# Optimization experiments

Measured on AMD Instinct MI355X. Metric: run time of the kernel, lower is better.

## Reference

```python
import jax, jax.numpy as jnp
import numpy as np

B, T, DIM, HEADS = 8, 1024, 256, 8
DH = DIM // HEADS


def setup_inputs() -> dict:
    key = jax.random.key(0)
    ks = jax.random.split(key, 8)
    x = jax.random.normal(ks[0], (B, T, DIM), dtype=jnp.float32)
    adj = jax.random.randint(ks[1], (B, 1, T, T), 0, 2).astype(jnp.int32)
    label = jax.random.randint(ks[2], (B,), 0, 10).astype(jnp.int64)
    Wq = jax.random.normal(ks[3], (DH, DH), dtype=jnp.float32) * 0.05
    Wk = jax.random.normal(ks[4], (DH, DH), dtype=jnp.float32) * 0.05
    Wv = jax.random.normal(ks[5], (DH, DH), dtype=jnp.float32) * 0.05
    Lam = jax.random.normal(ks[6], (HEADS, HEADS), dtype=jnp.float32)
    Wproj = jax.random.normal(ks[7], (DIM, DIM), dtype=jnp.float32) * 0.05
    return dict(x=x, adj=adj, label=label, Wq=Wq, Wk=Wk, Wv=Wv, Lam=Lam, Wproj=Wproj)


def reference(x, adj, label, Wq, Wk, Wv, Lam, Wproj):
    b, t, dim = x.shape
    h, dh = HEADS, dim // HEADS
    scale = dim ** (-0.5)  # note: scale uses full dim, as in the source
    # b t (h d) -> b h t d
    xh = x.reshape(b, t, h, dh).transpose(0, 2, 1, 3)
    adj_f = adj.astype(x.dtype)  # [b,1,t,t], broadcasts over heads

    def gcn(W, A):
        # graph conv: A @ (x @ W), per-head, weight shared across heads
        return jnp.matmul(A, jnp.einsum('bhtd,de->bhte', xh, W))

    q = gcn(Wq, adj_f)  # [b,h,t,dh]
    k = gcn(Wk, adj_f)
    attn = jnp.einsum('bhld,bhtd->bhlt', q, k) * scale
    attn = jax.nn.leaky_relu(attn, negative_slope=0.01)
    # cross-head Lambda mixing: new_head_i = sum_j Lam[i,j] * attn_head_j
    attn = jnp.einsum('ij,bjlt->bilt', Lam, attn)
    # layer_index=0 < depth//4=3 -> adjacency masking is active
    attn = jnp.where(adj > 0, attn, -jnp.inf)
    attn = jax.nn.softmax(attn, axis=-1)  # rep_adj [b,h,t,t]
    v = jnp.matmul(attn, jnp.einsum('bhtd,de->bhte', xh, Wv))  # GCN with attn as adjacency
    v = v.transpose(0, 2, 1, 3).reshape(b, t, dim)  # b h t d -> b t (h d)
    v = jax.nn.gelu(v, approximate=False)
    out = v @ Wproj.T  # nn.Linear, no bias
    return out, attn
```

## Files before the change

### kernel.cpp

```cpp
#include <hip/hip_runtime.h>
#include <cmath>

#define TT 1024
#define BB 8

typedef __attribute__((ext_vector_type(4))) float f4;
typedef __attribute__((ext_vector_type(4))) unsigned int u4;
typedef __attribute__((ext_vector_type(8))) short s8v;

__device__ __forceinline__ ushort f2bf(float x) {
  unsigned u = __builtin_bit_cast(unsigned, x);
  unsigned r = (u + 0x7FFFu + ((u >> 16) & 1u)) >> 16;
  return (ushort)r;
}
__device__ __forceinline__ float bf2f(ushort b) {
  unsigned u = ((unsigned)b) << 16;
  return __builtin_bit_cast(float, u);
}
__device__ __forceinline__ void st8(ushort* p, const ushort* v) {
  u4 w;
  w.x = (unsigned)v[0] | ((unsigned)v[1] << 16);
  w.y = (unsigned)v[2] | ((unsigned)v[3] << 16);
  w.z = (unsigned)v[4] | ((unsigned)v[5] << 16);
  w.w = (unsigned)v[6] | ((unsigned)v[7] << 16);
  *(u4*)p = w;
}

__global__ __launch_bounds__(256, 1) void k_xw(
    const float* __restrict__ x, const float* __restrict__ Wq,
    const float* __restrict__ Wk, const float* __restrict__ Wv,
    ushort* __restrict__ xTqhi, ushort* __restrict__ xTqlo,
    ushort* __restrict__ xTkhi, ushort* __restrict__ xTklo,
    ushort* __restrict__ vT) {
  __shared__ float xs[32][256];
  int bid = blockIdx.x;
  int b = bid & 7, t0 = (bid >> 3) * 32;
  int tid = threadIdx.x;
#pragma unroll
  for (int i = 0; i < 8; ++i) {
    int e = i * 256 + tid;
    int t = e >> 6, c4 = (e & 63) * 4;
    *(f4*)&xs[t][c4] = *(const f4*)&x[((size_t)(b * 1024 + t0 + t)) * 256 + c4];
  }
  int c = tid, h = c >> 5, d = c & 31;
  float wqr[32], wkr[32], wvr[32];
#pragma unroll
  for (int e = 0; e < 32; ++e) {
    wqr[e] = Wq[e * 32 + d] * 0.0625f;
    wkr[e] = Wk[e * 32 + d];
    wvr[e] = Wv[e * 32 + d];
  }
  __syncthreads();
  size_t rowq = ((size_t)(b * 256 + c)) * 1024 + t0;
#pragma unroll
  for (int tg = 0; tg < 4; ++tg) {
    ushort qh[8], ql[8], kh[8], kl[8], vh[8];
#pragma unroll
    for (int tt = 0; tt < 8; ++tt) {
      int t = tg * 8 + tt;
      float aq = 0.f, ak = 0.f, av = 0.f;
#pragma unroll
      for (int e = 0; e < 32; ++e) {
        float xe = xs[t][h * 32 + e];
        aq = fmaf(xe, wqr[e], aq);
        ak = fmaf(xe, wkr[e], ak);
        av = fmaf(xe, wvr[e], av);
      }
      ushort hq = f2bf(aq); qh[tt] = hq; ql[tt] = f2bf(aq - bf2f(hq));
      ushort hk = f2bf(ak); kh[tt] = hk; kl[tt] = f2bf(ak - bf2f(hk));
      vh[tt] = f2bf(av);
    }
    st8(xTqhi + rowq + tg * 8, qh);
    st8(xTqlo + rowq + tg * 8, ql);
    st8(xTkhi + rowq + tg * 8, kh);
    st8(xTklo + rowq + tg * 8, kl);
    st8(vT    + rowq + tg * 8, vh);
  }
}

__global__ __launch_bounds__(256, 1) void k_gcn(
    const int* __restrict__ adj,
    const ushort* __restrict__ xTqhi, const ushort* __restrict__ xTqlo,
    const ushort* __restrict__ xTkhi, const ushort* __restrict__ xTklo,
    ushort* __restrict__ qhi, ushort* __restrict__ qlo,
    ushort* __restrict__ khi, ushort* __restrict__ klo) {
  int bid = blockIdx.x;
  int b = bid & 7, r = bid >> 3;
  int lt = (r & 15) * 64, nt = r >> 4;
  const ushort* XH = (nt ? xTkhi : xTqhi) + (size_t)b * 256 * 1024;
  const ushort* XL = (nt ? xTklo : xTqlo) + (size_t)b * 256 * 1024;
  ushort* OH = (nt ? khi : qhi) + (size_t)b * 1024 * 256;
  ushort* OL = (nt ? klo : qlo) + (size_t)b * 1024 * 256;
  const int* AD = adj + (size_t)b * 1024 * 1024;
  int tid = threadIdx.x, wid = tid >> 6, lane = tid & 63;
  int lrow = lane & 15, lk = lane >> 4;
  int wr = wid >> 1, wc = wid & 1;
  int rbase = lt + wr * 32;
  int cbase = wc * 128;
  f4 acc[2][8];
#pragma unroll
  for (int i = 0; i < 2; ++i)
#pragma unroll
    for (int j = 0; j < 8; ++j) acc[i][j] = (f4)(0.f);

  for (int k0 = 0; k0 < 1024; k0 += 32) {
    s8v afr[2];
#pragma unroll
    for (int rq = 0; rq < 2; ++rq) {
      const int* ap = &AD[(size_t)(rbase + rq * 16 + lrow) * 1024 + k0 + lk * 8];
      int4 a0 = *(const int4*)ap;
      int4 a1 = *(const int4*)(ap + 4);
      u4 fw;
      fw.x = (a0.x ? 0x3F80u : 0u) | (a0.y ? 0x3F800000u : 0u);
      fw.y = (a0.z ? 0x3F80u : 0u) | (a0.w ? 0x3F800000u : 0u);
      fw.z = (a1.x ? 0x3F80u : 0u) | (a1.y ? 0x3F800000u : 0u);
      fw.w = (a1.z ? 0x3F80u : 0u) | (a1.w ? 0x3F800000u : 0u);
      afr[rq] = __builtin_bit_cast(s8v, fw);
    }
#pragma unroll
    for (int nq = 0; nq < 8; ++nq) {
      int col = cbase + nq * 16 + lrow;
      s8v bh = *(const s8v*)&XH[(size_t)col * 1024 + k0 + lk * 8];
      s8v bl = *(const s8v*)&XL[(size_t)col * 1024 + k0 + lk * 8];
#pragma unroll
      for (int rq = 0; rq < 2; ++rq) {
        acc[rq][nq] = __builtin_amdgcn_mfma_f32_16x16x32_bf16(afr[rq], bh, acc[rq][nq], 0, 0, 0);
        acc[rq][nq] = __builtin_amdgcn_mfma_f32_16x16x32_bf16(afr[rq], bl, acc[rq][nq], 0, 0, 0);
      }
    }
  }
#pragma unroll
  for (int rq = 0; rq < 2; ++rq)
#pragma unroll
    for (int nq = 0; nq < 8; ++nq)
#pragma unroll
      for (int e = 0; e < 4; ++e) {
        float v = acc[rq][nq][e];
        int row = rbase + rq * 16 + lk * 4 + e;
        int col = cbase + nq * 16 + lrow;
        ushort hi = f2bf(v);
        ushort lo = f2bf(v - bf2f(hi));
        OH[(size_t)row * 256 + col] = hi;
        OL[(size_t)row * 256 + col] = lo;
      }
}

__global__ __launch_bounds__(256, 1) void k_score(
    const ushort* __restrict__ qhi, const ushort* __restrict__ qlo,
    const ushort* __restrict__ khi, const ushort* __restrict__ klo,
    const int* __restrict__ adj, const float* __restrict__ Lam,
    float* __restrict__ attn) {
  __shared__ float sm_m[2][32][8];
  __shared__ float sm_s[2][32][8];
  __shared__ float fin_m[32][8];
  __shared__ float fin_r[32][8];
  int bid = blockIdx.x;
  int b = bid & 7, lt = (bid >> 3) * 32;
  int tid = threadIdx.x, wid = tid >> 6, lane = tid & 63;
  int lrow = lane & 15, lk = lane >> 4;
  int wr = wid >> 1, wc = wid & 1;
  const ushort* QH = qhi + (size_t)b * 1024 * 256;
  const ushort* QL = qlo + (size_t)b * 1024 * 256;
  const ushort* KH = khi + (size_t)b * 1024 * 256;
  const ushort* KL = klo + (size_t)b * 1024 * 256;
  const int* AD = adj + (size_t)b * 1024 * 1024;
  float* AT = attn + (size_t)b * 8 * 1024 * 1024;

  s8v qfh[8], qfl[8];
  int qrow = lt + wr * 16 + lrow;
#pragma unroll
  for (int h = 0; h < 8; ++h) {
    qfh[h] = *(const s8v*)&QH[(size_t)qrow * 256 + h * 32 + lk * 8];
    qfl[h] = *(const s8v*)&QL[(size_t)qrow * 256 + h * 32 + lk * 8];
  }
  float ms[4][8], ss[4][8];
#pragma unroll
  for (int e = 0; e < 4; ++e)
#pragma unroll
    for (int i2 = 0; i2 < 8; ++i2) { ms[e][i2] = -3.0e38f; ss[e][i2] = 0.f; }

  for (int it = 0; it < 32; ++it) {
    int t0 = (it * 2 + wc) * 16;
    f4 acc[8];
#pragma unroll
    for (int h = 0; h < 8; ++h) {
      s8v kh = *(const s8v*)&KH[(size_t)(t0 + lrow) * 256 + h * 32 + lk * 8];
      s8v kl = *(const s8v*)&KL[(size_t)(t0 + lrow) * 256 + h * 32 + lk * 8];
      f4 a = (f4)(0.f);
      a = __builtin_amdgcn_mfma_f32_16x16x32_bf16(qfh[h], kh, a, 0, 0, 0);
      a = __builtin_amdgcn_mfma_f32_16x16x32_bf16(qfh[h], kl, a, 0, 0, 0);
      a = __builtin_amdgcn_mfma_f32_16x16x32_bf16(qfl[h], kh, a, 0, 0, 0);
      acc[h] = a;
    }
#pragma unroll
    for (int e = 0; e < 4; ++e) {
      int row = lt + wr * 16 + lk * 4 + e;
      int a = AD[(size_t)row * 1024 + t0 + lrow];
      bool pred = a > 0;
      float raw[8];
#pragma unroll
      for (int h = 0; h < 8; ++h) { float v = acc[h][e]; raw[h] = fmaxf(v, 0.01f * v); }
#pragma unroll
      for (int i2 = 0; i2 < 8; ++i2) {
        float s = 0.f;
#pragma unroll
        for (int j = 0; j < 8; ++j) s = fmaf(Lam[i2 * 8 + j], raw[j], s);
        float d = s - ms[e][i2];
        float ex = __expf(fminf(d, -d));
        float snew = (d > 0.f) ? fmaf(ss[e][i2], ex, 1.f) : (ss[e][i2] + ex);
        float mnew = fmaxf(ms[e][i2], s);
        if (pred) { ss[e][i2] = snew; ms[e][i2] = mnew; }
      }
    }
  }
#pragma unroll
  for (int e = 0; e < 4; ++e)
#pragma unroll
    for (int i2 = 0; i2 < 8; ++i2) {
      float mm = ms[e][i2], sv = ss[e][i2];
      for (int off = 1; off < 16; off <<= 1) {
        float om = __shfl_xor(mm, off, 64);
        float os = __shfl_xor(sv, off, 64);
        float d = mm - om;
        float ex = __expf(fminf(d, -d));
        float sA = fmaf(os, ex, sv);
        float sB = fmaf(sv, ex, os);
        sv = (d >= 0.f) ? sA : sB;
        mm = fmaxf(mm, om);
      }
      ms[e][i2] = mm; ss[e][i2] = sv;
    }
  if (lrow == 0) {
#pragma unroll
    for (int e = 0; e < 4; ++e)
#pragma unroll
      for (int i2 = 0; i2 < 8; ++i2) {
        sm_m[wc][wr * 16 + lk * 4 + e][i2] = ms[e][i2];
        sm_s[wc][wr * 16 + lk * 4 + e][i2] = ss[e][i2];
      }
  }
  __syncthreads();
  {
    int rw = tid >> 3, i2 = tid & 7;
    float m0 = sm_m[0][rw][i2], m1 = sm_m[1][rw][i2];
    float s0 = sm_s[0][rw][i2], s1 = sm_s[1][rw][i2];
    float M = fmaxf(m0, m1);
    float S = s0 * __expf(m0 - M) + s1 * __expf(m1 - M);
    fin_m[rw][i2] = M;
    fin_r[rw][i2] = 1.f / S;
  }
  __syncthreads();
#pragma unroll
  for (int e = 0; e < 4; ++e)
#pragma unroll
    for (int i2 = 0; i2 < 8; ++i2) {
      ms[e][i2] = fin_m[wr * 16 + lk * 4 + e][i2];
      ss[e][i2] = fin_r[wr * 16 + lk * 4 + e][i2];
    }
  for (int it = 0; it < 32; ++it) {
    int t0 = (it * 2 + wc) * 16;
    f4 acc[8];
#pragma unroll
    for (int h = 0; h < 8; ++h) {
      s8v kh = *(const s8v*)&KH[(size_t)(t0 + lrow) * 256 + h * 32 + lk * 8];
      s8v kl = *(const s8v*)&KL[(size_t)(t0 + lrow) * 256 + h * 32 + lk * 8];
      f4 a = (f4)(0.f);
      a = __builtin_amdgcn_mfma_f32_16x16x32_bf16(qfh[h], kh, a, 0, 0, 0);
      a = __builtin_amdgcn_mfma_f32_16x16x32_bf16(qfh[h], kl, a, 0, 0, 0);
      a = __builtin_amdgcn_mfma_f32_16x16x32_bf16(qfl[h], kh, a, 0, 0, 0);
      acc[h] = a;
    }
#pragma unroll
    for (int e = 0; e < 4; ++e) {
      int row = lt + wr * 16 + lk * 4 + e;
      int a = AD[(size_t)row * 1024 + t0 + lrow];
      bool pred = a > 0;
      float raw[8];
#pragma unroll
      for (int h = 0; h < 8; ++h) { float v = acc[h][e]; raw[h] = fmaxf(v, 0.01f * v); }
#pragma unroll
      for (int i2 = 0; i2 < 8; ++i2) {
        float s = 0.f;
#pragma unroll
        for (int j = 0; j < 8; ++j) s = fmaf(Lam[i2 * 8 + j], raw[j], s);
        float p = pred ? __expf(s - ms[e][i2]) * ss[e][i2] : 0.f;
        AT[((size_t)i2 * 1024 + row) * 1024 + t0 + lrow] = p;
      }
    }
  }
}

__global__ __launch_bounds__(256, 4) void k_pv(
    const float* __restrict__ attn, const ushort* __restrict__ vT,
    float* __restrict__ g) {
  __shared__ ushort Vs[32][136];
  __shared__ unsigned pt[64 * 128 / 2];
  int bid = blockIdx.x;
  int b = bid & 7, h = (bid >> 3) & 7, lt = (bid >> 6) * 64;
  int tid = threadIdx.x, wid = tid >> 6, lane = tid & 63;
  int lrow = lane & 15, lk = lane >> 4;
  const float* AT = attn + ((size_t)(b * 8 + h) * 1024 + lt) * 1024;
  const ushort* VTb = vT + (size_t)(b * 256 + h * 32) * 1024;
  char* ptb = (char*)pt;
  f4 acc[2];
  acc[0] = (f4)(0.f); acc[1] = (f4)(0.f);

  for (int tc = 0; tc < 1024; tc += 128) {
    {
      int col = tid >> 3, toff = (tid & 7) * 16;
      u4 v0 = *(const u4*)&VTb[(size_t)col * 1024 + tc + toff];
      u4 v1 = *(const u4*)&VTb[(size_t)col * 1024 + tc + toff + 8];
      *(u4*)&Vs[col][toff] = v0;
      *(u4*)&Vs[col][toff + 8] = v1;
    }
    {
      int row = tid >> 2, tq = (tid & 3) * 32;
      const float* src = &AT[(size_t)row * 1024 + tc + tq];
#pragma unroll
      for (int i = 0; i < 4; ++i) {
        f4 p0 = *(const f4*)&src[i * 8];
        f4 p1 = *(const f4*)&src[i * 8 + 4];
        u4 pk;
        pk.x = (unsigned)f2bf(p0[0]) | ((unsigned)f2bf(p0[1]) << 16);
        pk.y = (unsigned)f2bf(p0[2]) | ((unsigned)f2bf(p0[3]) << 16);
        pk.z = (unsigned)f2bf(p1[0]) | ((unsigned)f2bf(p1[1]) << 16);
        pk.w = (unsigned)f2bf(p1[2]) | ((unsigned)f2bf(p1[3]) << 16);
        int t = tq + i * 8;
        int boff = row * 256 + ((t * 2) ^ ((row & 7) << 4));
        *(u4*)(ptb + boff) = pk;
      }
    }
    __syncthreads();
    int prow = wid * 16 + lrow;
#pragma unroll
    for (int ks = 0; ks < 4; ++ks) {
      int t = ks * 32 + lk * 8;
      int aoff = prow * 256 + ((t * 2) ^ ((prow & 7) << 4));
      s8v af = *(const s8v*)(ptb + aoff);
#pragma unroll
      for (int nq = 0; nq < 2; ++nq) {
        s8v bf = *(const s8v*)&Vs[nq * 16 + lrow][t];
        acc[nq] = __builtin_amdgcn_mfma_f32_16x16x32_bf16(af, bf, acc[nq], 0, 0, 0);
      }
    }
    __syncthreads();
  }
#pragma unroll
  for (int nq = 0; nq < 2; ++nq)
#pragma unroll
    for (int e = 0; e < 4; ++e) {
      float v = acc[nq][e];
      float ge = 0.5f * v * (1.f + erff(v * 0.70710678118654752f));
      int row = lt + wid * 16 + lk * 4 + e;
      int col = h * 32 + nq * 16 + lrow;
      g[(size_t)(b * 1024 + row) * 256 + col] = ge;
    }
}

__global__ __launch_bounds__(256) void k_proj(
    const float* __restrict__ g, const float* __restrict__ Wp,
    float* __restrict__ out) {
  __shared__ float g_s[16][68];
  __shared__ float w_s[16][68];
  int rt = blockIdx.y * 64;
  int it = blockIdx.x * 64;
  int tid = threadIdx.x;
  int tx = tid & 15, ty = tid >> 4;
  int r4 = tid >> 2, cq = tid & 3;
  float acc[4][4] = {};
  for (int kc = 0; kc < 256; kc += 16) {
    float4 gv = *(const float4*)&g[(size_t)(rt + r4) * 256 + kc + cq * 4];
    g_s[cq * 4 + 0][r4] = gv.x; g_s[cq * 4 + 1][r4] = gv.y;
    g_s[cq * 4 + 2][r4] = gv.z; g_s[cq * 4 + 3][r4] = gv.w;
    float4 wv = *(const float4*)&Wp[(size_t)(it + r4) * 256 + kc + cq * 4];
    w_s[cq * 4 + 0][r4] = wv.x; w_s[cq * 4 + 1][r4] = wv.y;
    w_s[cq * 4 + 2][r4] = wv.z; w_s[cq * 4 + 3][r4] = wv.w;
    __syncthreads();
#pragma unroll
    for (int k = 0; k < 16; ++k) {
      float4 a = *(const float4*)&g_s[k][ty * 4];
      float4 bb = *(const float4*)&w_s[k][tx * 4];
      acc[0][0] = fmaf(a.x, bb.x, acc[0][0]); acc[0][1] = fmaf(a.x, bb.y, acc[0][1]);
      acc[0][2] = fmaf(a.x, bb.z, acc[0][2]); acc[0][3] = fmaf(a.x, bb.w, acc[0][3]);
      acc[1][0] = fmaf(a.y, bb.x, acc[1][0]); acc[1][1] = fmaf(a.y, bb.y, acc[1][1]);
      acc[1][2] = fmaf(a.y, bb.z, acc[1][2]); acc[1][3] = fmaf(a.y, bb.w, acc[1][3]);
      acc[2][0] = fmaf(a.z, bb.x, acc[2][0]); acc[2][1] = fmaf(a.z, bb.y, acc[2][1]);
      acc[2][2] = fmaf(a.z, bb.z, acc[2][2]); acc[2][3] = fmaf(a.z, bb.w, acc[2][3]);
      acc[3][0] = fmaf(a.w, bb.x, acc[3][0]); acc[3][1] = fmaf(a.w, bb.y, acc[3][1]);
      acc[3][2] = fmaf(a.w, bb.z, acc[3][2]); acc[3][3] = fmaf(a.w, bb.w, acc[3][3]);
    }
    __syncthreads();
  }
#pragma unroll
  for (int i = 0; i < 4; ++i) {
    float4 o = make_float4(acc[i][0], acc[i][1], acc[i][2], acc[i][3]);
    *(float4*)&out[(size_t)(rt + ty * 4 + i) * 256 + it + tx * 4] = o;
  }
}

extern "C" void kernel_launch(void* const* d_in, const int* in_sizes, int n_in,
                              void* d_out, int out_size, void* d_ws, size_t ws_size,
                              hipStream_t stream) {
  const float* x   = (const float*)d_in[0];
  const int*   adj = (const int*)d_in[1];
  const float* Wq  = (const float*)d_in[3];
  const float* Wk  = (const float*)d_in[4];
  const float* Wv  = (const float*)d_in[5];
  const float* Lam = (const float*)d_in[6];
  const float* Wp  = (const float*)d_in[7];

  float* out  = (float*)d_out;
  float* attn = out + (size_t)BB * TT * 256;

  const size_t SZ = (size_t)8 * 1024 * 256;
  char* base = (char*)d_ws;
  ushort* xTqhi = (ushort*)(base + 0 * SZ * 2);
  ushort* xTqlo = (ushort*)(base + 1 * SZ * 2);
  ushort* xTkhi = (ushort*)(base + 2 * SZ * 2);
  ushort* xTklo = (ushort*)(base + 3 * SZ * 2);
  ushort* vT    = (ushort*)(base + 4 * SZ * 2);
  ushort* qhi   = (ushort*)(base + 5 * SZ * 2);
  ushort* qlo   = (ushort*)(base + 6 * SZ * 2);
  ushort* khi   = (ushort*)(base + 7 * SZ * 2);
  ushort* klo   = (ushort*)(base + 8 * SZ * 2);
  float*  gbuf  = (float*)(base + 9 * SZ * 2);

  k_xw<<<256, 256, 0, stream>>>(x, Wq, Wk, Wv, xTqhi, xTqlo, xTkhi, xTklo, vT);
  k_gcn<<<256, 256, 0, stream>>>(adj, xTqhi, xTqlo, xTkhi, xTklo, qhi, qlo, khi, klo);
  k_score<<<256, 256, 0, stream>>>(qhi, qlo, khi, klo, adj, Lam, attn);
  k_pv<<<1024, 256, 0, stream>>>(attn, vT, gbuf);
  k_proj<<<dim3(4, 128), 256, 0, stream>>>(gbuf, Wp, out);
}
```

Baseline: 515.9 us.

## Split score softmax across key chunks and widen GCN grid for occupancy

The score kernel is split into three launches: a per-key-chunk stats pass writing partial max/sum, a small reduce kernel combining eight partials per row, and a final pass that recomputes scores and writes normalized attention. This raises the grid from 256 to 2048 blocks so the GPU's compute units are better filled. The GCN kernel is also re-tiled to 512 blocks with half the columns per block. In exchange there are extra launches, workspace traffic for the partial statistics, and repeated Q fragment loads per chunk.

```diff
diff --git a/kernel.cpp b/kernel.cpp
--- a/kernel.cpp
+++ b/kernel.cpp
@@ -85,8 +85,8 @@
     ushort* __restrict__ qhi, ushort* __restrict__ qlo,
     ushort* __restrict__ khi, ushort* __restrict__ klo) {
   int bid = blockIdx.x;
-  int b = bid & 7, r = bid >> 3;
-  int lt = (r & 15) * 64, nt = r >> 4;
+  int ct = bid & 3, lt = ((bid >> 2) & 15) * 64, b = bid >> 6;
+  int nt = ct >> 1, cbase = (ct & 1) * 128;
   const ushort* XH = (nt ? xTkhi : xTqhi) + (size_t)b * 256 * 1024;
   const ushort* XL = (nt ? xTklo : xTqlo) + (size_t)b * 256 * 1024;
   ushort* OH = (nt ? khi : qhi) + (size_t)b * 1024 * 256;
@@ -96,12 +96,12 @@
   int lrow = lane & 15, lk = lane >> 4;
   int wr = wid >> 1, wc = wid & 1;
   int rbase = lt + wr * 32;
-  int cbase = wc * 128;
-  f4 acc[2][8];
+  int cb2 = cbase + wc * 64;
+  f4 acc[2][4];
 #pragma unroll
   for (int i = 0; i < 2; ++i)
 #pragma unroll
-    for (int j = 0; j < 8; ++j) acc[i][j] = (f4)(0.f);
+    for (int j = 0; j < 4; ++j) acc[i][j] = (f4)(0.f);
 
   for (int k0 = 0; k0 < 1024; k0 += 32) {
     s8v afr[2];
@@ -118,8 +118,8 @@
       afr[rq] = __builtin_bit_cast(s8v, fw);
     }
 #pragma unroll
-    for (int nq = 0; nq < 8; ++nq) {
-      int col = cbase + nq * 16 + lrow;
+    for (int nq = 0; nq < 4; ++nq) {
+      int col = cb2 + nq * 16 + lrow;
       s8v bh = *(const s8v*)&XH[(size_t)col * 1024 + k0 + lk * 8];
       s8v bl = *(const s8v*)&XL[(size_t)col * 1024 + k0 + lk * 8];
 #pragma unroll
@@ -132,12 +132,12 @@
 #pragma unroll
   for (int rq = 0; rq < 2; ++rq)
 #pragma unroll
-    for (int nq = 0; nq < 8; ++nq)
+    for (int nq = 0; nq < 4; ++nq)
 #pragma unroll
       for (int e = 0; e < 4; ++e) {
         float v = acc[rq][nq][e];
         int row = rbase + rq * 16 + lk * 4 + e;
-        int col = cbase + nq * 16 + lrow;
+        int col = cb2 + nq * 16 + lrow;
         ushort hi = f2bf(v);
         ushort lo = f2bf(v - bf2f(hi));
         OH[(size_t)row * 256 + col] = hi;
@@ -145,17 +145,17 @@
       }
 }
 
-__global__ __launch_bounds__(256, 1) void k_score(
+__global__ __launch_bounds__(256, 1) void k_stats(
     const ushort* __restrict__ qhi, const ushort* __restrict__ qlo,
     const ushort* __restrict__ khi, const ushort* __restrict__ klo,
     const int* __restrict__ adj, const float* __restrict__ Lam,
-    float* __restrict__ attn) {
+    float* __restrict__ pm, float* __restrict__ ps) {
   __shared__ float sm_m[2][32][8];
   __shared__ float sm_s[2][32][8];
-  __shared__ float fin_m[32][8];
-  __shared__ float fin_r[32][8];
   int bid = blockIdx.x;
-  int b = bid & 7, lt = (bid >> 3) * 32;
+  int b = bid >> 8;
+  int lt = ((bid >> 3) & 31) << 5;
+  int tc = bid & 7;
   int tid = threadIdx.x, wid = tid >> 6, lane = tid & 63;
   int lrow = lane & 15, lk = lane >> 4;
   int wr = wid >> 1, wc = wid & 1;
@@ -164,7 +164,6 @@
   const ushort* KH = khi + (size_t)b * 1024 * 256;
   const ushort* KL = klo + (size_t)b * 1024 * 256;
   const int* AD = adj + (size_t)b * 1024 * 1024;
-  float* AT = attn + (size_t)b * 8 * 1024 * 1024;
 
   s8v qfh[8], qfl[8];
   int qrow = lt + wr * 16 + lrow;
@@ -179,8 +178,8 @@
 #pragma unroll
     for (int i2 = 0; i2 < 8; ++i2) { ms[e][i2] = -3.0e38f; ss[e][i2] = 0.f; }
 
-  for (int it = 0; it < 32; ++it) {
-    int t0 = (it * 2 + wc) * 16;
+  for (int it = 0; it < 4; ++it) {
+    int t0 = tc * 128 + (it * 2 + wc) * 16;
     f4 acc[8];
 #pragma unroll
     for (int h = 0; h < 8; ++h) {
@@ -246,19 +245,75 @@
     float s0 = sm_s[0][rw][i2], s1 = sm_s[1][rw][i2];
     float M = fmaxf(m0, m1);
     float S = s0 * __expf(m0 - M) + s1 * __expf(m1 - M);
-    fin_m[rw][i2] = M;
-    fin_r[rw][i2] = 1.f / S;
+    size_t R = ((size_t)(b * 8 + i2) * 1024 + lt + rw);
+    pm[R * 8 + tc] = M;
+    ps[R * 8 + tc] = S;
+  }
+}
+
+__global__ __launch_bounds__(256) void k_reduce(
+    const float* __restrict__ pm, const float* __restrict__ ps,
+    float* __restrict__ fm, float* __restrict__ fr) {
+  int R = blockIdx.x * 256 + threadIdx.x;
+  f4 m0 = *(const f4*)&pm[(size_t)R * 8];
+  f4 m1 = *(const f4*)&pm[(size_t)R * 8 + 4];
+  f4 s0 = *(const f4*)&ps[(size_t)R * 8];
+  f4 s1 = *(const f4*)&ps[(size_t)R * 8 + 4];
+  float M = fmaxf(fmaxf(fmaxf(m0.x, m0.y), fmaxf(m0.z, m0.w)),
+                  fmaxf(fmaxf(m1.x, m1.y), fmaxf(m1.z, m1.w)));
+  float S = s0.x * __expf(m0.x - M) + s0.y * __expf(m0.y - M) +
+            s0.z * __expf(m0.z - M) + s0.w * __expf(m0.w - M) +
+            s1.x * __expf(m1.x - M) + s1.y * __expf(m1.y - M) +
+            s1.z * __expf(m1.z - M) + s1.w * __expf(m1.w - M);
+  fm[R] = M;
+  fr[R] = 1.f / S;
+}
+
+__global__ __launch_bounds__(256, 1) void k_final(
+    const ushort* __restrict__ qhi, const ushort* __restrict__ qlo,
+    const ushort* __restrict__ khi, const ushort* __restrict__ klo,
+    const int* __restrict__ adj, const float* __restrict__ Lam,
+    const float* __restrict__ fm, const float* __restrict__ fr,
+    float* __restrict__ attn) {
+  __shared__ float fin_m[32][8];
+  __shared__ float fin_r[32][8];
+  int bid = blockIdx.x;
+  int b = bid >> 8;
+  int lt = ((bid >> 3) & 31) << 5;
+  int tc = bid & 7;
+  int tid = threadIdx.x, wid = tid >> 6, lane = tid & 63;
+  int lrow = lane & 15, lk = lane >> 4;
+  int wr = wid >> 1, wc = wid & 1;
+  const ushort* QH = qhi + (size_t)b * 1024 * 256;
+  const ushort* QL = qlo + (size_t)b * 1024 * 256;
+  const ushort* KH = khi + (size_t)b * 1024 * 256;
+  const ushort* KL = klo + (size_t)b * 1024 * 256;
+  const int* AD = adj + (size_t)b * 1024 * 1024;
+  float* AT = attn + (size_t)b * 8 * 1024 * 1024;
+  {
+    int rw = tid >> 3, i2 = tid & 7;
+    size_t R = ((size_t)(b * 8 + i2) * 1024 + lt + rw);
+    fin_m[rw][i2] = fm[R];
+    fin_r[rw][i2] = fr[R];
+  }
+  s8v qfh[8], qfl[8];
+  int qrow = lt + wr * 16 + lrow;
+#pragma unroll
+  for (int h = 0; h < 8; ++h) {
+    qfh[h] = *(const s8v*)&QH[(size_t)qrow * 256 + h * 32 + lk * 8];
+    qfl[h] = *(const s8v*)&QL[(size_t)qrow * 256 + h * 32 + lk * 8];
   }
   __syncthreads();
+  float ms[4][8], rs[4][8];
 #pragma unroll
   for (int e = 0; e < 4; ++e)
 #pragma unroll
     for (int i2 = 0; i2 < 8; ++i2) {
       ms[e][i2] = fin_m[wr * 16 + lk * 4 + e][i2];
-      ss[e][i2] = fin_r[wr * 16 + lk * 4 + e][i2];
-    }
-  for (int it = 0; it < 32; ++it) {
-    int t0 = (it * 2 + wc) * 16;
+      rs[e][i2] = fin_r[wr * 16 + lk * 4 + e][i2];
+    }
+  for (int it = 0; it < 4; ++it) {
+    int t0 = tc * 128 + (it * 2 + wc) * 16;
     f4 acc[8];
 #pragma unroll
     for (int h = 0; h < 8; ++h) {
@@ -283,7 +338,7 @@
         float s = 0.f;
 #pragma unroll
         for (int j = 0; j < 8; ++j) s = fmaf(Lam[i2 * 8 + j], raw[j], s);
-        float p = pred ? __expf(s - ms[e][i2]) * ss[e][i2] : 0.f;
+        float p = pred ? __expf(s - ms[e][i2]) * rs[e][i2] : 0.f;
         AT[((size_t)i2 * 1024 + row) * 1024 + t0 + lrow] = p;
       }
     }
@@ -424,10 +479,16 @@
   ushort* khi   = (ushort*)(base + 7 * SZ * 2);
   ushort* klo   = (ushort*)(base + 8 * SZ * 2);
   float*  gbuf  = (float*)(base + 9 * SZ * 2);
+  float*  pm    = (float*)(base + 9 * SZ * 2 + SZ * 4);
+  float*  ps    = pm + 524288;
+  float*  fmb   = ps + 524288;
+  float*  frb   = fmb + 65536;
 
   k_xw<<<256, 256, 0, stream>>>(x, Wq, Wk, Wv, xTqhi, xTqlo, xTkhi, xTklo, vT);
-  k_gcn<<<256, 256, 0, stream>>>(adj, xTqhi, xTqlo, xTkhi, xTklo, qhi, qlo, khi, klo);
-  k_score<<<256, 256, 0, stream>>>(qhi, qlo, khi, klo, adj, Lam, attn);
+  k_gcn<<<512, 256, 0, stream>>>(adj, xTqhi, xTqlo, xTkhi, xTklo, qhi, qlo, khi, klo);
+  k_stats<<<2048, 256, 0, stream>>>(qhi, qlo, khi, klo, adj, Lam, pm, ps);
+  k_reduce<<<256, 256, 0, stream>>>(pm, ps, fmb, frb);
+  k_final<<<2048, 256, 0, stream>>>(qhi, qlo, khi, klo, adj, Lam, fmb, frb, attn);
   k_pv<<<1024, 256, 0, stream>>>(attn, vT, gbuf);
   k_proj<<<dim3(4, 128), 256, 0, stream>>>(gbuf, Wp, out);
 }
```

Result: no change. 515.0 us (-0.2%).
